# Performance work log

Hardware: AMD Instinct MI355X
Metric: run time of the kernel (lower is better)

The kernel has to match this reference:

```python
import jax, jax.numpy as jnp
import numpy as np

EPS = 1e-5
EXTEND_SCOPE = 1.0

def conv2d(x, w, b, pad):
    out = jax.lax.conv_general_dilated(x, w, (1, 1), [(pad, pad), (pad, pad)],
                                       dimension_numbers=('NCHW', 'OIHW', 'NCHW'))
    return out + b[None, :, None, None]

def group_norm(x, groups, gamma, beta):
    B, C, H, W = x.shape
    xg = x.reshape(B, groups, -1)
    mu = xg.mean(-1, keepdims=True)
    var = xg.var(-1, keepdims=True)
    xn = ((xg - mu) * jax.lax.rsqrt(var + EPS)).reshape(B, C, H, W)
    return xn * gamma[None, :, None, None] + beta[None, :, None, None]

def bilinear_sample(feat, y, x):
    # feat [B,C,H,W]; y,x pixel coords [B,Ho,Wo]; zeros padding, align_corners=True
    B, C, H, W = feat.shape
    flat = feat.reshape(B, C, H * W)
    y0 = jnp.floor(y); x0 = jnp.floor(x)
    wy = (y - y0)[:, None]; wx = (x - x0)[:, None]  # [B,1,Ho,Wo]
    y0i = y0.astype(jnp.int32); x0i = x0.astype(jnp.int32)
    Ho, Wo = y.shape[1], y.shape[2]
    def gather(yi, xi):
        valid = ((yi >= 0) & (yi < H) & (xi >= 0) & (xi < W)).astype(feat.dtype)[:, None]
        idx = (jnp.clip(yi, 0, H - 1) * W + jnp.clip(xi, 0, W - 1)).reshape(B, -1)
        g = jax.vmap(lambda f, i: f[:, i])(flat, idx).reshape(B, C, Ho, Wo)
        return g * valid
    g00 = gather(y0i, x0i)
    g01 = gather(y0i, x0i + 1)
    g10 = gather(y0i + 1, x0i)
    g11 = gather(y0i + 1, x0i + 1)
    return g00 * (1 - wy) * (1 - wx) + g01 * (1 - wy) * wx + g10 * wy * (1 - wx) + g11 * wy * wx

def setup_inputs() -> dict:
    key = jax.random.key(0)
    ks = jax.random.split(key, 4)
    B, C, H, W, K, O = 4, 64, 128, 128, 9, 64
    return {
        'x': jax.random.normal(ks[0], (B, C, H, W), jnp.float32),
        'w_off': jax.random.normal(ks[1], (K, C, 3, 3), jnp.float32) * 0.05,
        'b_off': jnp.zeros((K,), jnp.float32),
        'w_theta': jax.random.normal(ks[2], (K, C, 5, 5), jnp.float32) * 0.05,
        'b_theta': jnp.zeros((K,), jnp.float32),
        'gn_off_g': jnp.ones((K,), jnp.float32),
        'gn_off_b': jnp.zeros((K,), jnp.float32),
        'gn_th_g': jnp.ones((K,), jnp.float32),
        'gn_th_b': jnp.zeros((K,), jnp.float32),
        'w_strip': jax.random.normal(ks[3], (O, C, K, 1), jnp.float32) * 0.05,
        'b_strip': jnp.zeros((O,), jnp.float32),
        'gn_out_g': jnp.ones((O,), jnp.float32),
        'gn_out_b': jnp.zeros((O,), jnp.float32),
    }

def reference(x, w_off, b_off, w_theta, b_theta, gn_off_g, gn_off_b,
              gn_th_g, gn_th_b, w_strip, b_strip, gn_out_g, gn_out_b):
    B, C, H, W = x.shape
    K = w_off.shape[0]
    center = K // 2
    off = jnp.tanh(group_norm(conv2d(x, w_off, b_off, 1), 3, gn_off_g, gn_off_b))       # [B,K,H,W]
    th = jnp.arctan(group_norm(conv2d(x, w_theta, b_theta, 2), 3, gn_th_g, gn_th_b))    # [B,K,H,W]
    k = jnp.arange(K)
    s = (k - center).astype(x.dtype)[None, :, None, None]   # signed kernel offset
    m = center + jnp.abs(k - center)                        # mirror index (uses theta/offset at center+|i|)
    th_m = th[:, m]; off_m = off[:, m]                      # [B,K,H,W]
    is_center = (k == center)[None, :, None, None]
    y_off = jnp.where(is_center, 0.0, s * jnp.tan(th_m) + off_m * jnp.cos(th_m))
    x_off = jnp.where(is_center, 0.0, s - jnp.sin(th_m) * off_m)
    y_new = jnp.arange(H, dtype=x.dtype)[None, None, :, None] + s + EXTEND_SCOPE * y_off
    x_new = jnp.arange(W, dtype=x.dtype)[None, None, None, :] + s + EXTEND_SCOPE * x_off
    # rearrange 'b k h w -> b (h k) w'
    y_map = y_new.transpose(0, 2, 1, 3).reshape(B, H * K, W)
    x_map = x_new.transpose(0, 2, 1, 3).reshape(B, H * K, W)
    # clamp to valid range; scale to [-1,1] + align_corners=True grid_sample is identity in pixel space
    y_map = jnp.clip(y_map, 0.0, float(H - 1))
    x_map = jnp.clip(x_map, 0.0, float(W - 1))
    deformed = bilinear_sample(x, y_map, x_map)             # [B,C,K*H,W]
    d = deformed.reshape(B, C, H, K, W)
    out = jnp.einsum('bchkw,ock->bohw', d, w_strip[..., 0]) + b_strip[None, :, None, None]
    O = w_strip.shape[0]
    out = jax.nn.relu(group_norm(out, O // 4, gn_out_g, gn_out_b))
    return out
```

## Files before the change

### kernel.cpp

```cpp
#include <hip/hip_runtime.h>
#include <math.h>


typedef short v8s __attribute__((ext_vector_type(8)));
typedef float v4f __attribute__((ext_vector_type(4)));

__device__ __forceinline__ float fast_tanh(float a) {
    float aa = fabsf(a);
    float e = __expf(2.f * aa);
    float t = 1.f - 2.f / (e + 1.f);
    return copysignf(t, a);
}

__device__ __forceinline__ float bf2f(short s) {
    union { unsigned u; float f; } v;
    v.u = ((unsigned)(unsigned short)s) << 16;
    return v.f;
}

__global__ __launch_bounds__(256) void k_pack(
    const float* __restrict__ w_strip, short* __restrict__ w_pack)
{
    int idx = blockIdx.x * 256 + threadIdx.x;
    int j    = idx & 7;
    int lane = (idx >> 3) & 63;
    int kk   = (idx >> 9) & 1;
    int og   = (idx >> 10) & 3;
    int k    = idx >> 12;
    int c = (kk << 5) + ((lane >> 4) << 3) + j;
    int o = (og << 4) + (lane & 15);
    union { short s; __bf16 h; } u;
    u.h = (__bf16)w_strip[(o * 64 + c) * 9 + k];
    w_pack[idx] = u.s;
}

__global__ __launch_bounds__(256) void k_tr(
    const float* __restrict__ x, short* __restrict__ xt)
{
    __shared__ float l[64][65];
    const int t    = threadIdx.x;
    const int lane = t & 63;
    const int wv   = t >> 6;
    const int b    = blockIdx.x >> 8;
    const int pix0 = (blockIdx.x & 255) << 6;

#pragma unroll
    for (int it = 0; it < 16; ++it) {
        int c = (wv << 4) + it;
        l[lane][c] = x[(((size_t)(b << 6) + c) << 14) + pix0 + lane];
    }
    __syncthreads();
    {
        const int p   = t >> 2;
        const int c16 = (t & 3) << 4;
        union { v8s s8; __bf16 hh[8]; } u0, u1;
#pragma unroll
        for (int j = 0; j < 8; ++j) {
            u0.hh[j] = (__bf16)l[p][c16 + j];
            u1.hh[j] = (__bf16)l[p][c16 + 8 + j];
        }
        short* dst = xt + (((size_t)(b << 14) + pix0 + p) << 6) + c16;
        *(v8s*)dst = u0.s8;
        *(v8s*)(dst + 8) = u1.s8;
    }
}

__global__ __launch_bounds__(256, 4) void k_conv(
    const float* __restrict__ x,
    const float* __restrict__ w_off, const float* __restrict__ b_off,
    const float* __restrict__ w_th,  const float* __restrict__ b_th,
    float* __restrict__ off_raw, float* __restrict__ th_raw)
{
    __shared__ float tile[12][36];
    const int t  = threadIdx.x;
    const int tx = t & 31, ty = t >> 5;
    const int z  = blockIdx.z;
    const int b  = z >> 2, sp = z & 3;
    const int c0 = sp << 4;
    const int h0 = blockIdx.y << 3, w0 = blockIdx.x << 5;

    const int r1 = t / 36,        cc1 = t - r1 * 36;
    const int e2 = t + 256;
    const int r2 = e2 / 36,       cc2 = e2 - r2 * 36;
    const int hh1 = h0 + r1 - 2,  ww1 = w0 + cc1 - 2;
    const int hh2 = h0 + r2 - 2,  ww2 = w0 + cc2 - 2;
    const bool va1 = (hh1 >= 0 && hh1 < 128 && ww1 >= 0 && ww1 < 128);
    const bool va2 = (t < 176) && (hh2 >= 0 && hh2 < 128 && ww2 >= 0 && ww2 < 128);
    const int of1 = (hh1 << 7) + ww1;
    const int of2 = (hh2 << 7) + ww2;
    const float* xb = x + (((size_t)(b << 6) + c0) << 14);

    float accO[9], accT[9];
#pragma unroll
    for (int k = 0; k < 9; ++k) { accO[k] = 0.f; accT[k] = 0.f; }

    float ra = va1 ? xb[of1] : 0.f;
    float rb = va2 ? xb[of2] : 0.f;

    for (int ci = 0; ci < 16; ++ci) {
        const int c = c0 + ci;
        __builtin_amdgcn_sched_barrier(0);
        asm volatile("s_waitcnt lgkmcnt(0)" ::: "memory");
        __builtin_amdgcn_s_barrier();
        __builtin_amdgcn_sched_barrier(0);

        tile[r1][cc1] = ra;
        if (t < 176) tile[r2][cc2] = rb;

        if (ci < 15) {
            const float* xp = xb + ((size_t)(ci + 1) << 14);
            ra = va1 ? xp[of1] : 0.f;
            rb = va2 ? xp[of2] : 0.f;
        }

        __builtin_amdgcn_sched_barrier(0);
        asm volatile("s_waitcnt lgkmcnt(0)" ::: "memory");
        __builtin_amdgcn_s_barrier();
        __builtin_amdgcn_sched_barrier(0);

        float win[5][5];
#pragma unroll
        for (int i = 0; i < 5; ++i)
#pragma unroll
            for (int j = 0; j < 5; ++j)
                win[i][j] = tile[ty + i][tx + j];

#pragma unroll
        for (int k = 0; k < 9; ++k) {
            const float* wo = w_off + (size_t)((k << 6) + c) * 9;
            float a = accO[k];
#pragma unroll
            for (int i = 0; i < 3; ++i)
#pragma unroll
                for (int j = 0; j < 3; ++j)
                    a = fmaf(win[i + 1][j + 1], wo[i * 3 + j], a);
            accO[k] = a;

            const float* wt = w_th + (size_t)((k << 6) + c) * 25;
            float bb = accT[k];
#pragma unroll
            for (int i = 0; i < 5; ++i)
#pragma unroll
                for (int j = 0; j < 5; ++j)
                    bb = fmaf(win[i][j], wt[i * 5 + j], bb);
            accT[k] = bb;
        }
    }

    const int pix = ((h0 + ty) << 7) + (w0 + tx);
#pragma unroll
    for (int k = 0; k < 9; ++k) {
        float vo = accO[k] + (sp == 0 ? b_off[k] : 0.f);
        float vt = accT[k] + (sp == 0 ? b_th[k]  : 0.f);
        atomicAdd(&off_raw[((b * 9 + k) << 14) + pix], vo);
        atomicAdd(&th_raw [((b * 9 + k) << 14) + pix], vt);
    }
}

__global__ __launch_bounds__(256) void k_stats(
    const float* __restrict__ off_raw, const float* __restrict__ th_raw,
    float* __restrict__ stats)
{
    const int id  = blockIdx.x;
    const int arr = id >= 36;
    const int rem = id - arr * 36;
    const float4* src = (const float4*)((arr ? th_raw : off_raw) + (rem << 14));

    float s1 = 0.f, s2 = 0.f;
    for (int i = threadIdx.x; i < 4096; i += 256) {
        float4 v = src[i];
        s1 += v.x + v.y + v.z + v.w;
        s2 += v.x * v.x + v.y * v.y + v.z * v.z + v.w * v.w;
    }
#pragma unroll
    for (int d = 32; d; d >>= 1) { s1 += __shfl_down(s1, d, 64); s2 += __shfl_down(s2, d, 64); }

    __shared__ float ls1[4], ls2[4];
    const int wv = threadIdx.x >> 6;
    if ((threadIdx.x & 63) == 0) { ls1[wv] = s1; ls2[wv] = s2; }
    __syncthreads();
    if (threadIdx.x == 0) {
        stats[arr * 72 + rem]      = ls1[0] + ls1[1] + ls1[2] + ls1[3];
        stats[arr * 72 + 36 + rem] = ls2[0] + ls2[1] + ls2[2] + ls2[3];
    }
}

__global__ __launch_bounds__(256, 4) void k_sample_strip3(
    const short* __restrict__ xt,
    const float* __restrict__ off_raw, const float* __restrict__ th_raw,
    const float* __restrict__ stats,
    const float* __restrict__ g_off, const float* __restrict__ be_off,
    const float* __restrict__ g_th,  const float* __restrict__ be_th,
    const short* __restrict__ w_pack, const float* __restrict__ b_strip,
    float* __restrict__ out, float* __restrict__ out_stats)
{
    __shared__ __align__(16) short smem[2][2048];
    const int t    = threadIdx.x;
    const int lane = t & 63;
    const int wv   = __builtin_amdgcn_readfirstlane(t >> 6);
    const int bid  = blockIdx.x;
    const int blk  = ((bid & 7) << 8) + (bid >> 3);
    const int b    = blk >> 9;
    const int pix0 = (blk & 511) << 5;
    const int l32  = lane & 31;
    const int q    = lane >> 5;
    const int p_img = pix0 + l32;
    const int h    = p_img >> 7, w = p_img & 127;
    const int i15  = lane & 15, lg = lane >> 4;
    const int cg   = (wv << 4) + (q << 3);
    const int cb   = (wv << 1) + q;

    const float inv_cnt = 1.f / (3.f * 16384.f);
    float muO1, isO1, muT1, isT1, muO2, isO2, muT2, isT2;
    {
        float s, qq, mu;
        s = stats[b*9+3] + stats[b*9+4] + stats[b*9+5];
        qq = stats[36+b*9+3] + stats[36+b*9+4] + stats[36+b*9+5];
        mu = s * inv_cnt; muO1 = mu;
        isO1 = rsqrtf(fmaxf(qq * inv_cnt - mu * mu, 0.f) + 1e-5f);
        s = stats[b*9+6] + stats[b*9+7] + stats[b*9+8];
        qq = stats[36+b*9+6] + stats[36+b*9+7] + stats[36+b*9+8];
        mu = s * inv_cnt; muO2 = mu;
        isO2 = rsqrtf(fmaxf(qq * inv_cnt - mu * mu, 0.f) + 1e-5f);
        s = stats[72+b*9+3] + stats[72+b*9+4] + stats[72+b*9+5];
        qq = stats[108+b*9+3] + stats[108+b*9+4] + stats[108+b*9+5];
        mu = s * inv_cnt; muT1 = mu;
        isT1 = rsqrtf(fmaxf(qq * inv_cnt - mu * mu, 0.f) + 1e-5f);
        s = stats[72+b*9+6] + stats[72+b*9+7] + stats[72+b*9+8];
        qq = stats[108+b*9+6] + stats[108+b*9+7] + stats[108+b*9+8];
        mu = s * inv_cnt; muT2 = mu;
        isT2 = rsqrtf(fmaxf(qq * inv_cnt - mu * mu, 0.f) + 1e-5f);
    }

    float zt[4], cyv[4], cxv[4];
#pragma unroll
    for (int m = 5; m <= 8; ++m) {
        const int mi = m - 5;
        float tv = th_raw [((b * 9 + m) << 14) + p_img];
        float ov = off_raw[((b * 9 + m) << 14) + p_img];
        float muT = (m == 5) ? muT1 : muT2, isT = (m == 5) ? isT1 : isT2;
        float muO = (m == 5) ? muO1 : muO2, isO = (m == 5) ? isO1 : isO2;
        float z = (tv - muT) * isT * g_th[m] + be_th[m];
        float f = fast_tanh((ov - muO) * isO * g_off[m] + be_off[m]);
        float r = rsqrtf(1.f + z * z);
        zt[mi]  = z;
        cyv[mi] = f * r;
        cxv[mi] = z * r * f;
    }

    const short* xtb = xt + ((size_t)b << 20);

    auto coords = [&](int k, float& cwy, float& cwx) -> int {
        const int s  = k - 4;
        const int mi = (s < 0 ? -s : s) - 1;
        const float fs = (float)s;
        float yy = (float)h + fs + fs * zt[mi] + cyv[mi];
        float xx = (float)w + 2.f * fs - cxv[mi];
        yy = fminf(fmaxf(yy, 0.f), 127.f);
        xx = fminf(fmaxf(xx, 0.f), 127.f);
        int y0 = min((int)yy, 126), x0 = min((int)xx, 126);
        cwy = yy - (float)y0; cwx = xx - (float)x0;
        return (y0 << 7) + x0;
    };

    v8s Gb[2][4];
    v8s Af[2][2];
    float wyv[2], wxv[2];

    auto issueG = [&](int k) {
        if (k == 4) {
            const short* bb = xtb + ((size_t)p_img << 6) + cg;
            Gb[k & 1][0] = *(const v8s*)bb;
        } else {
            int cidx = coords(k, wyv[k & 1], wxv[k & 1]);
            const short* bb = xtb + ((size_t)cidx << 6) + cg;
            Gb[k & 1][0] = *(const v8s*)bb;
            Gb[k & 1][1] = *(const v8s*)(bb + 64);
            Gb[k & 1][2] = *(const v8s*)(bb + 8192);
            Gb[k & 1][3] = *(const v8s*)(bb + 8256);
        }
    };
    auto issueA = [&](int k) {
        const short* wa = w_pack + (((k << 2) + wv) << 10) + (lane << 3);
        Af[k & 1][0] = *(const v8s*)wa;
        Af[k & 1][1] = *(const v8s*)(wa + 512);
    };

    issueG(0); issueA(0);
    issueG(1); issueA(1);

    v4f acc[2];
    acc[0] = (v4f)0.f; acc[1] = (v4f)0.f;

#pragma unroll
    for (int k = 0; k < 9; ++k) {
        float vj[8];
        if (k == 4) {
#pragma unroll
            for (int j = 0; j < 8; ++j) vj[j] = bf2f(Gb[k & 1][0][j]);
        } else {
            const float cwy = wyv[k & 1], cwx = wxv[k & 1];
#pragma unroll
            for (int j = 0; j < 8; ++j) {
                float c00 = bf2f(Gb[k & 1][0][j]), c01 = bf2f(Gb[k & 1][1][j]);
                float c10 = bf2f(Gb[k & 1][2][j]), c11 = bf2f(Gb[k & 1][3][j]);
                float top = fmaf(cwx, c01 - c00, c00);
                float bot = fmaf(cwx, c11 - c10, c10);
                vj[j] = fmaf(cwy, bot - top, top);
            }
        }

        if (k < 7) issueG(k + 2);

        union { v8s s8; __bf16 hh[8]; } u;
#pragma unroll
        for (int j = 0; j < 8; ++j) u.hh[j] = (__bf16)vj[j];
        *(v8s*)&smem[k & 1][((cb << 5) + l32) << 3] = u.s8;

        __builtin_amdgcn_sched_barrier(0);
        asm volatile("s_waitcnt lgkmcnt(0)" ::: "memory");
        __builtin_amdgcn_s_barrier();
        __builtin_amdgcn_sched_barrier(0);

#pragma unroll
        for (int n = 0; n < 2; ++n) {
            int p16 = (n << 4) + i15;
            v8s b0 = *(const v8s*)&smem[k & 1][((lg << 5) + p16) << 3];
            v8s b1 = *(const v8s*)&smem[k & 1][(((lg + 4) << 5) + p16) << 3];
            acc[n] = __builtin_amdgcn_mfma_f32_16x16x32_bf16(Af[k & 1][0], b0, acc[n], 0, 0, 0);
            acc[n] = __builtin_amdgcn_mfma_f32_16x16x32_bf16(Af[k & 1][1], b1, acc[n], 0, 0, 0);
        }

        if (k < 7) issueA(k + 2);
    }

#pragma unroll
    for (int r = 0; r < 4; ++r) {
        int o = (wv << 4) + (lg << 2) + r;
        float bias = b_strip[o];
        float v0 = acc[0][r] + bias;
        float v1 = acc[1][r] + bias;
        float* op = out + (((size_t)(b << 6) + o) << 14) + pix0 + i15;
        op[0]  = v0;
        op[16] = v1;
        float s1 = v0 + v1;
        float s2 = v0 * v0 + v1 * v1;
#pragma unroll
        for (int d = 1; d <= 8; d <<= 1) {
            s1 += __shfl_xor(s1, d, 64);
            s2 += __shfl_xor(s2, d, 64);
        }
        if (i15 == 0) {
            atomicAdd(&out_stats[(b << 6) + o], s1);
            atomicAdd(&out_stats[256 + (b << 6) + o], s2);
        }
    }
}

__global__ __launch_bounds__(256) void k_sample_strip_old(
    const float* __restrict__ x,
    const float* __restrict__ off_raw, const float* __restrict__ th_raw,
    const float* __restrict__ stats,
    const float* __restrict__ g_off, const float* __restrict__ be_off,
    const float* __restrict__ g_th,  const float* __restrict__ be_th,
    const short* __restrict__ w_pack, const float* __restrict__ b_strip,
    float* __restrict__ out)
{
    __shared__ __align__(16) short smem[64 * 64];
    const int t    = threadIdx.x;
    const int lane = t & 63;
    const int wv   = __builtin_amdgcn_readfirstlane(t >> 6);
    const int bid  = blockIdx.x;
    const int blk  = ((bid & 7) << 7) + (bid >> 3);
    const int b    = blk >> 8;
    const int pix0 = (blk & 255) << 6;
    const int p    = pix0 + lane;
    const int h    = p >> 7, w = p & 127;
    const int i15  = lane & 15, lg = lane >> 4;

    float muO[3], isO[3], muT[3], isT[3];
    const float inv_cnt = 1.f / (3.f * 16384.f);
#pragma unroll
    for (int g = 0; g < 3; ++g) {
        float s = 0.f, q = 0.f;
#pragma unroll
        for (int j = 0; j < 3; ++j) { s += stats[b * 9 + 3 * g + j]; q += stats[36 + b * 9 + 3 * g + j]; }
        float mu = s * inv_cnt;
        muO[g] = mu; isO[g] = rsqrtf(fmaxf(q * inv_cnt - mu * mu, 0.f) + 1e-5f);
        s = 0.f; q = 0.f;
#pragma unroll
        for (int j = 0; j < 3; ++j) { s += stats[72 + b * 9 + 3 * g + j]; q += stats[108 + b * 9 + 3 * g + j]; }
        mu = s * inv_cnt;
        muT[g] = mu; isT[g] = rsqrtf(fmaxf(q * inv_cnt - mu * mu, 0.f) + 1e-5f);
    }

    const float* xb = x + ((size_t)((b << 6) + (wv << 4)) << 14);
    v4f acc[4];
#pragma unroll
    for (int n = 0; n < 4; ++n) acc[n] = (v4f)0.f;

    for (int k = 0; k < 9; ++k) {
        float v[16];
        if (k == 4) {
#pragma unroll
            for (int ci = 0; ci < 16; ++ci) v[ci] = xb[(ci << 14) + p];
        } else {
            const int s = k - 4;
            const int m = 4 + (s < 0 ? -s : s);
            const int g = m / 3;
            float z = (th_raw[((b * 9 + m) << 14) + p] - muT[g]) * isT[g] * g_th[m] + be_th[m];
            float f = fast_tanh((off_raw[((b * 9 + m) << 14) + p] - muO[g]) * isO[g] * g_off[m] + be_off[m]);
            float r = rsqrtf(1.f + z * z);
            float fs = (float)s;
            float yy = (float)h + fs + fs * z + f * r;
            float xx = (float)w + fs + fs - z * r * f;
            yy = fminf(fmaxf(yy, 0.f), 127.f);
            xx = fminf(fmaxf(xx, 0.f), 127.f);
            int y0 = min((int)yy, 126);
            int x0 = min((int)xx, 126);
            float wy = yy - (float)y0;
            float wx = xx - (float)x0;
            const float* base = xb + (y0 << 7) + x0;
#pragma unroll
            for (int ci = 0; ci < 16; ++ci) {
                const float* qp = base + (ci << 14);
                float2 r0 = *(const float2*)qp;
                float2 r1 = *(const float2*)(qp + 128);
                float lo = fmaf(wx, r0.y - r0.x, r0.x);
                float hi = fmaf(wx, r1.y - r1.x, r1.x);
                v[ci] = fmaf(wy, hi - lo, lo);
            }
        }

        union { v8s s8; __bf16 hh[8]; } u0, u1;
#pragma unroll
        for (int ci = 0; ci < 8; ++ci) { u0.hh[ci] = (__bf16)v[ci]; u1.hh[ci] = (__bf16)v[ci + 8]; }
        *(v8s*)&smem[(lane << 6) + ((((wv << 1) + 0) + lane) & 7) * 8] = u0.s8;
        *(v8s*)&smem[(lane << 6) + ((((wv << 1) + 1) + lane) & 7) * 8] = u1.s8;
        __syncthreads();

        const short* wpk = w_pack + (((k << 2) + wv) << 10) + (lane << 3);
        v8s a0 = *(const v8s*)wpk;
        v8s a1 = *(const v8s*)(wpk + 512);

#pragma unroll
        for (int n = 0; n < 4; ++n) {
            int r = (n << 4) + i15;
            v8s b0 = *(const v8s*)&smem[(r << 6) + (((lg    ) + r) & 7) * 8];
            v8s b1 = *(const v8s*)&smem[(r << 6) + (((lg + 4) + r) & 7) * 8];
            acc[n] = __builtin_amdgcn_mfma_f32_16x16x32_bf16(a0, b0, acc[n], 0, 0, 0);
            acc[n] = __builtin_amdgcn_mfma_f32_16x16x32_bf16(a1, b1, acc[n], 0, 0, 0);
        }
        __syncthreads();
    }

#pragma unroll
    for (int r = 0; r < 4; ++r) {
        int o = (wv << 4) + (lg << 2) + r;
        float bias = b_strip[o];
        float* op = out + ((size_t)((b << 6) + o) << 14) + pix0 + i15;
#pragma unroll
        for (int n = 0; n < 4; ++n)
            op[n << 4] = acc[n][r] + bias;
    }
}

__global__ __launch_bounds__(256) void k_stats_out(
    const float* __restrict__ out, float* __restrict__ out_stats)
{
    const int bo = blockIdx.x;
    const float4* src = (const float4*)(out + ((size_t)bo << 14));
    float s1 = 0.f, s2 = 0.f;
    for (int i = threadIdx.x; i < 4096; i += 256) {
        float4 v = src[i];
        s1 += v.x + v.y + v.z + v.w;
        s2 += v.x * v.x + v.y * v.y + v.z * v.z + v.w * v.w;
    }
#pragma unroll
    for (int d = 32; d; d >>= 1) { s1 += __shfl_down(s1, d, 64); s2 += __shfl_down(s2, d, 64); }

    __shared__ float ls1[4], ls2[4];
    const int wv = threadIdx.x >> 6;
    if ((threadIdx.x & 63) == 0) { ls1[wv] = s1; ls2[wv] = s2; }
    __syncthreads();
    if (threadIdx.x == 0) {
        out_stats[bo]       = ls1[0] + ls1[1] + ls1[2] + ls1[3];
        out_stats[256 + bo] = ls2[0] + ls2[1] + ls2[2] + ls2[3];
    }
}

__global__ __launch_bounds__(256) void k_gn_out(
    float* __restrict__ out, const float* __restrict__ out_stats,
    const float* __restrict__ gg, const float* __restrict__ gb)
{
    const float inv_cnt = 1.f / (4.f * 16384.f);
    const int n4 = 1 << 20;
    for (int idx = blockIdx.x * 256 + threadIdx.x; idx < n4; idx += gridDim.x * 256) {
        int flat = idx << 2;
        int ch = (flat >> 14) & 63;
        int b  = flat >> 20;
        int cb = (b << 6) + ((ch >> 2) << 2);
        float s = out_stats[cb] + out_stats[cb + 1] + out_stats[cb + 2] + out_stats[cb + 3];
        float q = out_stats[256 + cb] + out_stats[256 + cb + 1] + out_stats[256 + cb + 2] + out_stats[256 + cb + 3];
        float mu   = s * inv_cnt;
        float istd = rsqrtf(fmaxf(q * inv_cnt - mu * mu, 0.f) + 1e-5f);
        float ga = gg[ch] * istd;
        float be = gb[ch] - mu * ga;
        float4 v = *reinterpret_cast<float4*>(out + flat);
        v.x = fmaxf(fmaf(v.x, ga, be), 0.f);
        v.y = fmaxf(fmaf(v.y, ga, be), 0.f);
        v.z = fmaxf(fmaf(v.z, ga, be), 0.f);
        v.w = fmaxf(fmaf(v.w, ga, be), 0.f);
        *reinterpret_cast<float4*>(out + flat) = v;
    }
}

extern "C" void kernel_launch(void* const* d_in, const int* in_sizes, int n_in,
                              void* d_out, int out_size, void* d_ws, size_t ws_size,
                              hipStream_t stream)
{
    const float* x       = (const float*)d_in[0];
    const float* w_off   = (const float*)d_in[1];
    const float* b_off   = (const float*)d_in[2];
    const float* w_th    = (const float*)d_in[3];
    const float* b_th    = (const float*)d_in[4];
    const float* g_off   = (const float*)d_in[5];
    const float* be_off  = (const float*)d_in[6];
    const float* g_th    = (const float*)d_in[7];
    const float* be_th   = (const float*)d_in[8];
    const float* w_strip = (const float*)d_in[9];
    const float* b_strip = (const float*)d_in[10];
    const float* gg      = (const float*)d_in[11];
    const float* gb      = (const float*)d_in[12];

    float* out       = (float*)d_out;
    float* ws        = (float*)d_ws;
    float* off_raw   = ws;
    float* th_raw    = ws + 589824;
    float* stats     = ws + 1179648;
    float* out_stats = ws + 1179792;
    short* w_pack    = (short*)(ws + 1180304);
    short* xt        = (short*)(ws + 1198736);

    const size_t need_full = (size_t)(1198736 + 2097152) * sizeof(float);
    const bool big = ws_size >= need_full;

    hipMemsetAsync(ws, 0, (size_t)1180304 * sizeof(float), stream);

    k_pack<<<144, 256, 0, stream>>>(w_strip, w_pack);
    if (big) k_tr<<<1024, 256, 0, stream>>>(x, xt);
    dim3 g1(4, 16, 16);
    k_conv<<<g1, 256, 0, stream>>>(x, w_off, b_off, w_th, b_th, off_raw, th_raw);
    k_stats<<<72, 256, 0, stream>>>(off_raw, th_raw, stats);
    if (big) {
        k_sample_strip3<<<2048, 256, 0, stream>>>(xt, off_raw, th_raw, stats,
                                                  g_off, be_off, g_th, be_th,
                                                  w_pack, b_strip, out, out_stats);
    } else {
        k_sample_strip_old<<<1024, 256, 0, stream>>>(x, off_raw, th_raw, stats,
                                                     g_off, be_off, g_th, be_th,
                                                     w_pack, b_strip, out);
        k_stats_out<<<256, 256, 0, stream>>>(out, out_stats);
    }
    k_gn_out<<<4096, 256, 0, stream>>>(out, out_stats, gg, gb);
}
```

Baseline: 174.9 us.

## Fuse GroupNorm stats into full-channel conv and drop channel-split atomics

The offset/theta conv kernel now loops over all 64 input channels per block instead of splitting channels four ways. It writes raw outputs directly instead of using atomicAdd, which removes the large workspace memset, and only the small stats region is still cleared. Per-group sum and sum-of-squares are reduced with wave shuffles inside the conv epilogue, replacing the separate stats kernel. The LDS tile is double-buffered so each channel step needs one barrier instead of two, and the sampling kernel raises wave priority around its MFMA block. The trade-off is a grid a quarter the size with launch bounds of one block, which lowers the occupancy available to hide latency in the conv.

```diff
diff --git a/kernel.cpp b/kernel.cpp
--- a/kernel.cpp
+++ b/kernel.cpp
@@ -65,18 +65,17 @@
     }
 }
 
-__global__ __launch_bounds__(256, 4) void k_conv(
+__global__ __launch_bounds__(256, 1) void k_conv(
     const float* __restrict__ x,
     const float* __restrict__ w_off, const float* __restrict__ b_off,
     const float* __restrict__ w_th,  const float* __restrict__ b_th,
-    float* __restrict__ off_raw, float* __restrict__ th_raw)
-{
-    __shared__ float tile[12][36];
+    float* __restrict__ off_raw, float* __restrict__ th_raw,
+    float* __restrict__ stats)
+{
+    __shared__ float tile[2][12][36];
     const int t  = threadIdx.x;
     const int tx = t & 31, ty = t >> 5;
-    const int z  = blockIdx.z;
-    const int b  = z >> 2, sp = z & 3;
-    const int c0 = sp << 4;
+    const int b  = blockIdx.z;
     const int h0 = blockIdx.y << 3, w0 = blockIdx.x << 5;
 
     const int r1 = t / 36,        cc1 = t - r1 * 36;
@@ -88,7 +87,7 @@
     const bool va2 = (t < 176) && (hh2 >= 0 && hh2 < 128 && ww2 >= 0 && ww2 < 128);
     const int of1 = (hh1 << 7) + ww1;
     const int of2 = (hh2 << 7) + ww2;
-    const float* xb = x + (((size_t)(b << 6) + c0) << 14);
+    const float* xb = x + ((size_t)(b << 6) << 14);
 
     float accO[9], accT[9];
 #pragma unroll
@@ -97,33 +96,28 @@
     float ra = va1 ? xb[of1] : 0.f;
     float rb = va2 ? xb[of2] : 0.f;
 
-    for (int ci = 0; ci < 16; ++ci) {
-        const int c = c0 + ci;
+    for (int c = 0; c < 64; ++c) {
+        const int buf = c & 1;
+        tile[buf][r1][cc1] = ra;
+        if (t < 176) tile[buf][r2][cc2] = rb;
+
+        if (c < 63) {
+            const float* xp = xb + ((size_t)(c + 1) << 14);
+            ra = va1 ? xp[of1] : 0.f;
+            rb = va2 ? xp[of2] : 0.f;
+        }
+
         __builtin_amdgcn_sched_barrier(0);
         asm volatile("s_waitcnt lgkmcnt(0)" ::: "memory");
         __builtin_amdgcn_s_barrier();
         __builtin_amdgcn_sched_barrier(0);
 
-        tile[r1][cc1] = ra;
-        if (t < 176) tile[r2][cc2] = rb;
-
-        if (ci < 15) {
-            const float* xp = xb + ((size_t)(ci + 1) << 14);
-            ra = va1 ? xp[of1] : 0.f;
-            rb = va2 ? xp[of2] : 0.f;
-        }
-
-        __builtin_amdgcn_sched_barrier(0);
-        asm volatile("s_waitcnt lgkmcnt(0)" ::: "memory");
-        __builtin_amdgcn_s_barrier();
-        __builtin_amdgcn_sched_barrier(0);
-
         float win[5][5];
 #pragma unroll
         for (int i = 0; i < 5; ++i)
 #pragma unroll
             for (int j = 0; j < 5; ++j)
-                win[i][j] = tile[ty + i][tx + j];
+                win[i][j] = tile[buf][ty + i][tx + j];
 
 #pragma unroll
         for (int k = 0; k < 9; ++k) {
@@ -150,38 +144,24 @@
     const int pix = ((h0 + ty) << 7) + (w0 + tx);
 #pragma unroll
     for (int k = 0; k < 9; ++k) {
-        float vo = accO[k] + (sp == 0 ? b_off[k] : 0.f);
-        float vt = accT[k] + (sp == 0 ? b_th[k]  : 0.f);
-        atomicAdd(&off_raw[((b * 9 + k) << 14) + pix], vo);
-        atomicAdd(&th_raw [((b * 9 + k) << 14) + pix], vt);
-    }
-}
-
-__global__ __launch_bounds__(256) void k_stats(
-    const float* __restrict__ off_raw, const float* __restrict__ th_raw,
-    float* __restrict__ stats)
-{
-    const int id  = blockIdx.x;
-    const int arr = id >= 36;
-    const int rem = id - arr * 36;
-    const float4* src = (const float4*)((arr ? th_raw : off_raw) + (rem << 14));
-
-    float s1 = 0.f, s2 = 0.f;
-    for (int i = threadIdx.x; i < 4096; i += 256) {
-        float4 v = src[i];
-        s1 += v.x + v.y + v.z + v.w;
-        s2 += v.x * v.x + v.y * v.y + v.z * v.z + v.w * v.w;
-    }
-#pragma unroll
-    for (int d = 32; d; d >>= 1) { s1 += __shfl_down(s1, d, 64); s2 += __shfl_down(s2, d, 64); }
-
-    __shared__ float ls1[4], ls2[4];
-    const int wv = threadIdx.x >> 6;
-    if ((threadIdx.x & 63) == 0) { ls1[wv] = s1; ls2[wv] = s2; }
-    __syncthreads();
-    if (threadIdx.x == 0) {
-        stats[arr * 72 + rem]      = ls1[0] + ls1[1] + ls1[2] + ls1[3];
-        stats[arr * 72 + 36 + rem] = ls2[0] + ls2[1] + ls2[2] + ls2[3];
+        float vo = accO[k] + b_off[k];
+        float vt = accT[k] + b_th[k];
+        off_raw[((b * 9 + k) << 14) + pix] = vo;
+        th_raw [((b * 9 + k) << 14) + pix] = vt;
+        float s1 = vo, s2 = vo * vo, s3 = vt, s4 = vt * vt;
+#pragma unroll
+        for (int d = 32; d; d >>= 1) {
+            s1 += __shfl_down(s1, d, 64);
+            s2 += __shfl_down(s2, d, 64);
+            s3 += __shfl_down(s3, d, 64);
+            s4 += __shfl_down(s4, d, 64);
+        }
+        if ((t & 63) == 0) {
+            atomicAdd(&stats[      b * 9 + k], s1);
+            atomicAdd(&stats[ 36 + b * 9 + k], s2);
+            atomicAdd(&stats[ 72 + b * 9 + k], s3);
+            atomicAdd(&stats[108 + b * 9 + k], s4);
+        }
     }
 }
 
@@ -322,6 +302,7 @@
         __builtin_amdgcn_s_barrier();
         __builtin_amdgcn_sched_barrier(0);
 
+        __builtin_amdgcn_s_setprio(1);
 #pragma unroll
         for (int n = 0; n < 2; ++n) {
             int p16 = (n << 4) + i15;
@@ -330,6 +311,7 @@
             acc[n] = __builtin_amdgcn_mfma_f32_16x16x32_bf16(Af[k & 1][0], b0, acc[n], 0, 0, 0);
             acc[n] = __builtin_amdgcn_mfma_f32_16x16x32_bf16(Af[k & 1][1], b1, acc[n], 0, 0, 0);
         }
+        __builtin_amdgcn_s_setprio(0);
 
         if (k < 7) issueA(k + 2);
     }
@@ -545,13 +527,13 @@
     const size_t need_full = (size_t)(1198736 + 2097152) * sizeof(float);
     const bool big = ws_size >= need_full;
 
-    hipMemsetAsync(ws, 0, (size_t)1180304 * sizeof(float), stream);
+    hipMemsetAsync(stats, 0, 656 * sizeof(float), stream);
 
     k_pack<<<144, 256, 0, stream>>>(w_strip, w_pack);
     if (big) k_tr<<<1024, 256, 0, stream>>>(x, xt);
-    dim3 g1(4, 16, 16);
-    k_conv<<<g1, 256, 0, stream>>>(x, w_off, b_off, w_th, b_th, off_raw, th_raw);
-    k_stats<<<72, 256, 0, stream>>>(off_raw, th_raw, stats);
+    dim3 g1(4, 16, 4);
+    k_conv<<<g1, 256, 0, stream>>>(x, w_off, b_off, w_th, b_th,
+                                   off_raw, th_raw, stats);
     if (big) {
         k_sample_strip3<<<2048, 256, 0, stream>>>(xt, off_raw, th_raw, stats,
                                                   g_off, be_off, g_th, be_th,
```

Measured after the change: 384.7 us. 2.2x slower.
